# Kernel tuning notes

Measured on AMD Instinct MI355X. Metric: run time of the kernel, lower is better.

The kernel has to match this reference:

```python
import jax, jax.numpy as jnp
import numpy as np

DETER, STOCH, ACT, HID, OBS = 1024, 32, 6, 1024, 1024
B, T = 256, 64

def _lin(x, w, b):
    return x @ w.T + b

def setup_inputs() -> dict:
    key = jax.random.key(0)
    ks = iter(jax.random.split(key, 40))
    def p(shape, scale=0.02):
        return (jax.random.normal(next(ks), shape, dtype=jnp.float32) * scale)
    inp = {
        "obs": jax.random.normal(next(ks), (B, T, OBS), dtype=jnp.float32),
        "actions": jax.random.normal(next(ks), (B, T, ACT), dtype=jnp.float32),
        "eps_prior": jax.random.normal(next(ks), (B, T, STOCH), dtype=jnp.float32),
        "eps_post": jax.random.normal(next(ks), (B, T, STOCH), dtype=jnp.float32),
        # input_mlp
        "in_w1": p((HID, STOCH + ACT)), "in_b1": p((HID,)),
        "in_w2": p((HID, HID)), "in_b2": p((HID,)),
        # GRUCell (torch layout: r,z,n chunks)
        "gru_wih": p((3 * DETER, HID)), "gru_whh": p((3 * DETER, DETER)),
        "gru_bih": p((3 * DETER,)), "gru_bhh": p((3 * DETER,)),
        # prior
        "pr_w1": p((HID, DETER)), "pr_b1": p((HID,)),
        "pr_w2": p((HID, HID)), "pr_b2": p((HID,)),
        "pr_mw": p((STOCH, HID)), "pr_mb": p((STOCH,)),
        "pr_sw": p((STOCH, HID)), "pr_sb": p((STOCH,)),
        # posterior
        "po_w1": p((HID, DETER + OBS)), "po_b1": p((HID,)),
        "po_w2": p((HID, HID)), "po_b2": p((HID,)),
        "po_mw": p((STOCH, HID)), "po_mb": p((STOCH,)),
        "po_sw": p((STOCH, HID)), "po_sb": p((STOCH,)),
    }
    return inp

def _rollout(obs, actions, eps_prior, eps_post,
             in_w1, in_b1, in_w2, in_b2,
             gru_wih, gru_whh, gru_bih, gru_bhh,
             pr_w1, pr_b1, pr_w2, pr_b2, pr_mw, pr_mb, pr_sw, pr_sb,
             po_w1, po_b1, po_w2, po_b2, po_mw, po_mb, po_sw, po_sb):
    Bn = obs.shape[0]
    h0 = jnp.zeros((Bn, DETER), obs.dtype)
    z0 = jnp.zeros((Bn, STOCH), obs.dtype)
    a0 = jnp.zeros((Bn, ACT), obs.dtype)

    def step(carry, xs):
        h, z, prev_a = carry
        obs_t, act_t, ep, eq = xs
        x = jnp.concatenate([z, prev_a], axis=-1)
        x = jax.nn.relu(_lin(x, in_w1, in_b1))
        x = jax.nn.relu(_lin(x, in_w2, in_b2))
        # GRUCell
        gi = _lin(x, gru_wih, gru_bih)
        gh = _lin(h, gru_whh, gru_bhh)
        ir, iz, inn = jnp.split(gi, 3, axis=-1)
        hr, hz, hn = jnp.split(gh, 3, axis=-1)
        r = jax.nn.sigmoid(ir + hr)
        u = jax.nn.sigmoid(iz + hz)
        n = jnp.tanh(inn + r * hn)
        h_new = (1.0 - u) * n + u * h
        # prior
        px = jax.nn.relu(_lin(h_new, pr_w1, pr_b1))
        px = jax.nn.relu(_lin(px, pr_w2, pr_b2))
        p_mean = _lin(px, pr_mw, pr_mb)
        p_std = jnp.exp(jnp.clip(_lin(px, pr_sw, pr_sb), -5.0, 2.0))
        # posterior
        qx = jnp.concatenate([h_new, obs_t], axis=-1)
        qx = jax.nn.relu(_lin(qx, po_w1, po_b1))
        qx = jax.nn.relu(_lin(qx, po_w2, po_b2))
        q_mean = _lin(qx, po_mw, po_mb)
        q_std = jnp.exp(jnp.clip(_lin(qx, po_sw, po_sb), -5.0, 2.0))
        z_new = q_mean + q_std * eq
        feat = jnp.concatenate([h_new, z_new], axis=-1)
        return (h_new, z_new, act_t), (feat, p_mean, p_std, q_mean, q_std)

    xs = (jnp.swapaxes(obs, 0, 1), jnp.swapaxes(actions, 0, 1),
          jnp.swapaxes(eps_prior, 0, 1), jnp.swapaxes(eps_post, 0, 1))
    _, (feat, pm, ps, qm, qs) = jax.lax.scan(step, (h0, z0, a0), xs)
    to_bt = lambda a: jnp.swapaxes(a, 0, 1)  # [T,B,...] -> [B,T,...]
    return to_bt(feat), to_bt(pm), to_bt(ps), to_bt(qm), to_bt(qs)

def reference(obs, actions, eps_prior, eps_post,
              in_w1, in_b1, in_w2, in_b2,
              gru_wih, gru_whh, gru_bih, gru_bhh,
              pr_w1, pr_b1, pr_w2, pr_b2, pr_mw, pr_mb, pr_sw, pr_sb,
              po_w1, po_b1, po_w2, po_b2, po_mw, po_mb, po_sw, po_sb):
    return _rollout(obs, actions, eps_prior, eps_post,
                    in_w1, in_b1, in_w2, in_b2,
                    gru_wih, gru_whh, gru_bih, gru_bhh,
                    pr_w1, pr_b1, pr_w2, pr_b2, pr_mw, pr_mb, pr_sw, pr_sb,
                    po_w1, po_b1, po_w2, po_b2, po_mw, po_mb, po_sw, po_sb)
```

## Files before the change

### kernel.cpp

```cpp
#include <hip/hip_runtime.h>
#include <hip/hip_bf16.h>

#define B_   256
#define T_   64
#define OBS_ 1024
#define ACT_ 6
#define STO_ 32
#define HID_ 1024

using bf16 = __bf16;
typedef __attribute__((ext_vector_type(8))) __bf16 bf16x8;
typedef __attribute__((ext_vector_type(4))) float f32x4;

__device__ __forceinline__ f32x4 MF(bf16x8 a, bf16x8 b, f32x4 c) {
  return __builtin_amdgcn_mfma_f32_16x16x32_bf16(a, b, c, 0, 0, 0);
}

struct CvtArgs {
  const float *in_w2, *gru_wih, *gru_whh, *pr_w1, *pr_w2, *po_w1, *po_w2;
  const float *pr_mw, *pr_sw, *po_mw, *po_sw, *obs;
  bf16 *w_in2b, *w_wihb, *w_whhb, *w_pr1b, *w_pr2b, *w_po1hb, *w_po1ob, *w_po2b, *w_headb, *obsb;
};

__global__ void k_cvtall(CvtArgs a) {
  const int row = blockIdx.x;
  const float* src; bf16* dst;
  if      (row < 1024)  { src = a.in_w2   + (size_t)row * 1024;               dst = a.w_in2b  + (size_t)row * 1024; }
  else if (row < 4096)  { int r = row - 1024;  src = a.gru_wih + (size_t)r * 1024;        dst = a.w_wihb  + (size_t)r * 1024; }
  else if (row < 7168)  { int r = row - 4096;  src = a.gru_whh + (size_t)r * 1024;        dst = a.w_whhb  + (size_t)r * 1024; }
  else if (row < 8192)  { int r = row - 7168;  src = a.pr_w1   + (size_t)r * 1024;        dst = a.w_pr1b  + (size_t)r * 1024; }
  else if (row < 9216)  { int r = row - 8192;  src = a.pr_w2   + (size_t)r * 1024;        dst = a.w_pr2b  + (size_t)r * 1024; }
  else if (row < 10240) { int r = row - 9216;  src = a.po_w1   + (size_t)r * 2048;        dst = a.w_po1hb + (size_t)r * 1024; }
  else if (row < 11264) { int r = row - 10240; src = a.po_w1   + (size_t)r * 2048 + 1024; dst = a.w_po1ob + (size_t)r * 1024; }
  else if (row < 12288) { int r = row - 11264; src = a.po_w2   + (size_t)r * 1024;        dst = a.w_po2b  + (size_t)r * 1024; }
  else if (row < 12416) {
    int r = row - 12288;
    const float* hs[4] = { a.pr_mw, a.pr_sw, a.po_mw, a.po_sw };
    src = hs[r >> 5] + (size_t)(r & 31) * 1024;
    dst = a.w_headb + (size_t)r * 1024;
  }
  else { int r = row - 12416; src = a.obs + (size_t)r * 1024; dst = a.obsb + (size_t)r * 1024; }
  const int c = threadIdx.x * 4;
  float4 f = *(const float4*)(src + c);
  dst[c] = (bf16)f.x; dst[c + 1] = (bf16)f.y; dst[c + 2] = (bf16)f.z; dst[c + 3] = (bf16)f.w;
}

__global__ void k_init(const float* __restrict__ in_b1, bf16* __restrict__ x1b,
                       bf16* __restrict__ hbA, bf16* __restrict__ hbB,
                       float* __restrict__ hfA, float* __restrict__ hfB) {
  const int i = blockIdx.x * 256 + threadIdx.x;
  x1b[i] = (bf16)fmaxf(in_b1[i & 1023], 0.f);
  hbA[i] = (bf16)0.f; hbB[i] = (bf16)0.f;
  hfA[i] = 0.f; hfB[i] = 0.f;
}

struct GB2 {
  const bf16 *A1, *A2, *W1, *W2;
  const float* bias;
  bf16* out;
  int lda1, lda2, K1, kseg;
};

__global__ __launch_bounds__(256, 4) void k_l1(GB2 g0, GB2 g1, int s1) {
  GB2 g; int tile;
  if ((int)blockIdx.x < s1) { g = g0; tile = blockIdx.x; }
  else                      { g = g1; tile = blockIdx.x - s1; }
  __shared__ float sh[3 * 1056];
  const int tid = threadIdx.x, lane = tid & 63, kw = tid >> 6;
  const int l15 = lane & 15, kg = lane >> 4, kq = kg * 8, rq = kg * 4;
  const int m0 = (tile & 15) * 16, n0 = (tile >> 4) * 64;
  const int kb = kw * g.kseg;

  const bf16* __restrict__ ap;
  const bf16* __restrict__ wp;
  if (kb < g.K1) {
    ap = g.A1 + (size_t)(m0 + l15) * g.lda1 + kb + kq;
    wp = g.W1 + (size_t)(n0 + l15) * 1024 + kb + kq;
  } else {
    ap = g.A2 + (size_t)(m0 + l15) * g.lda2 + (kb - g.K1) + kq;
    wp = g.W2 + (size_t)(n0 + l15) * 1024 + (kb - g.K1) + kq;
  }
  f32x4 c0{0.f,0.f,0.f,0.f}, c1 = c0, c2 = c0, c3 = c0;
  #pragma unroll 8
  for (int k = 0; k < g.kseg; k += 32) {
    bf16x8 af = *(const bf16x8*)(ap + k);
    c0 = MF(af, *(const bf16x8*)(wp + k            ), c0);
    c1 = MF(af, *(const bf16x8*)(wp + 16 * 1024 + k), c1);
    c2 = MF(af, *(const bf16x8*)(wp + 32 * 1024 + k), c2);
    c3 = MF(af, *(const bf16x8*)(wp + 48 * 1024 + k), c3);
  }
  f32x4 cc[4] = {c0, c1, c2, c3};
  if (kw) {
    float* s = sh + (kw - 1) * 1056;
    #pragma unroll
    for (int t2 = 0; t2 < 4; ++t2)
      #pragma unroll
      for (int r = 0; r < 4; ++r)
        s[(rq + r) * 66 + t2 * 16 + l15] = cc[t2][r];
  }
  __syncthreads();
  if (kw == 0) {
    #pragma unroll
    for (int t2 = 0; t2 < 4; ++t2) {
      const int n = n0 + t2 * 16 + l15;
      const float bv = g.bias[n];
      #pragma unroll
      for (int r = 0; r < 4; ++r) {
        float v = cc[t2][r] + bv;
        #pragma unroll
        for (int s = 0; s < 3; ++s)
          v += sh[s * 1056 + (rq + r) * 66 + t2 * 16 + l15];
        g.out[(size_t)(m0 + rq + r) * 1024 + n] = (bf16)fmaxf(v, 0.f);
      }
    }
  }
}

__global__ __launch_bounds__(512, 2) void k_gru(
    const bf16* __restrict__ hbPrev, const float* __restrict__ hfPrev,
    bf16* __restrict__ hbCur, float* __restrict__ hfCur,
    const bf16* __restrict__ x2b, const bf16* __restrict__ wih,
    const bf16* __restrict__ whh, const float* __restrict__ bih,
    const float* __restrict__ bhh, float* __restrict__ feat, int t) {
  __shared__ float sh[4 * 1088];
  const int mt = blockIdx.x & 3, cs = blockIdx.x >> 2;
  const int tid = threadIdx.x, lane = tid & 63, wv = tid >> 6;
  const int msub = wv & 3, kw = wv >> 2;
  const int l15 = lane & 15, kg = lane >> 4, kq = kg * 8, rq = kg * 4;
  const int mrow = mt * 64 + msub * 16;
  const int c0 = cs * 16;
  const int kb = kw * 512;
  const size_t GOFF = (size_t)1024 * 1024;

  f32x4 ghR{0.f,0.f,0.f,0.f}, ghZ = ghR, ghN = ghR, giR = ghR, giZ = ghR, giN = ghR;
  {
    const bf16* __restrict__ ap = hbPrev + (size_t)(mrow + l15) * 1024 + kb + kq;
    const bf16* __restrict__ wr = whh + (size_t)(c0 + l15) * 1024 + kb + kq;
    #pragma unroll 4
    for (int k = 0; k < 512; k += 32) {
      bf16x8 af = *(const bf16x8*)(ap + k);
      ghR = MF(af, *(const bf16x8*)(wr + k           ), ghR);
      ghZ = MF(af, *(const bf16x8*)(wr + GOFF + k    ), ghZ);
      ghN = MF(af, *(const bf16x8*)(wr + 2 * GOFF + k), ghN);
    }
  }
  {
    const bf16* __restrict__ ap = x2b + (size_t)(mrow + l15) * 1024 + kb + kq;
    const bf16* __restrict__ wr = wih + (size_t)(c0 + l15) * 1024 + kb + kq;
    #pragma unroll 4
    for (int k = 0; k < 512; k += 32) {
      bf16x8 af = *(const bf16x8*)(ap + k);
      giR = MF(af, *(const bf16x8*)(wr + k           ), giR);
      giZ = MF(af, *(const bf16x8*)(wr + GOFF + k    ), giZ);
      giN = MF(af, *(const bf16x8*)(wr + 2 * GOFF + k), giN);
    }
  }
  f32x4 sR = ghR + giR, sZ = ghZ + giZ;
  if (kw) {
    float* s = sh + msub * 1088;
    #pragma unroll
    for (int r = 0; r < 4; ++r) {
      s[      (rq + r) * 17 + l15] = sR[r];
      s[272 + (rq + r) * 17 + l15] = sZ[r];
      s[544 + (rq + r) * 17 + l15] = giN[r];
      s[816 + (rq + r) * 17 + l15] = ghN[r];
    }
  }
  __syncthreads();
  if (kw == 0) {
    const int c = c0 + l15;
    const float bir = bih[c], biz = bih[1024 + c], bin_ = bih[2048 + c];
    const float bhr = bhh[c], bhz = bhh[1024 + c], bhn = bhh[2048 + c];
    const float* s = sh + msub * 1088;
    #pragma unroll
    for (int r = 0; r < 4; ++r) {
      const float vr  = sR[r]  + s[      (rq + r) * 17 + l15];
      const float vz  = sZ[r]  + s[272 + (rq + r) * 17 + l15];
      const float vin = giN[r] + s[544 + (rq + r) * 17 + l15];
      const float vhn = ghN[r] + s[816 + (rq + r) * 17 + l15];
      const int row = mrow + rq + r;
      float rr = vr + bir + bhr;
      float zz = vz + biz + bhz;
      rr = 1.f / (1.f + __expf(-rr));
      zz = 1.f / (1.f + __expf(-zz));
      const float nn = tanhf(vin + bin_ + rr * (vhn + bhn));
      const float h2 = (1.f - zz) * nn + zz * hfPrev[(size_t)row * 1024 + c];
      hbCur[(size_t)row * 1024 + c] = (bf16)h2;
      hfCur[(size_t)row * 1024 + c] = h2;
      feat[((size_t)row * T_ + t) * 1056 + c] = h2;
    }
  }
}

__global__ __launch_bounds__(1024, 1) void k_fin3(
    const bf16* __restrict__ p2b, const bf16* __restrict__ q2b,
    const bf16* __restrict__ whead, const bf16* __restrict__ win2,
    const float* __restrict__ pr_mb, const float* __restrict__ pr_sb,
    const float* __restrict__ po_mb, const float* __restrict__ po_sb,
    const float* __restrict__ b_in2,
    const float* __restrict__ eps, const float* __restrict__ act,
    const float* __restrict__ in_w1, const float* __restrict__ in_b1,
    float* __restrict__ pm, float* __restrict__ ps,
    float* __restrict__ qm, float* __restrict__ qs,
    float* __restrict__ feat, bf16* __restrict__ x2b, int t) {
  __shared__ float sh[12288];
  const int g = blockIdx.x >> 3, nt = blockIdx.x & 7, m0 = g * 16;
  const int tid = threadIdx.x, lane = tid & 63, wv = tid >> 6;
  const int l15 = lane & 15, kg = lane >> 4, kq = kg * 8, rq = kg * 4;
  float* zm = sh + 8448;
  float* zs = sh + 8960;
  float* zl = sh + 9472;
  float* al = sh + 9984;
  float* shE = sh + 10112;

  if (wv < 8) {
    const int kw = wv & 3, half = wv >> 2;
    const bf16* __restrict__ A = half ? q2b : p2b;
    f32x4 c0{0.f,0.f,0.f,0.f}, c1 = c0, c2 = c0, c3 = c0;
    const bf16* __restrict__ ap = A + (size_t)(m0 + l15) * 1024 + kw * 256 + kq;
    const bf16* __restrict__ wp = whead + (size_t)(half * 64 + l15) * 1024 + kw * 256 + kq;
    #pragma unroll
    for (int k = 0; k < 256; k += 32) {
      bf16x8 af = *(const bf16x8*)(ap + k);
      c0 = MF(af, *(const bf16x8*)(wp + k            ), c0);
      c1 = MF(af, *(const bf16x8*)(wp + 16 * 1024 + k), c1);
      c2 = MF(af, *(const bf16x8*)(wp + 32 * 1024 + k), c2);
      c3 = MF(af, *(const bf16x8*)(wp + 48 * 1024 + k), c3);
    }
    f32x4 cc[4] = {c0, c1, c2, c3};
    float* s = sh + wv * 1056;
    #pragma unroll
    for (int t2 = 0; t2 < 4; ++t2)
      #pragma unroll
      for (int r = 0; r < 4; ++r)
        s[(rq + r) * 66 + t2 * 16 + l15] = cc[t2][r];
  }
  if (tid >= 928 && tid < 1024) {
    const int idx = tid - 928, r = idx / ACT_, k = idx - r * ACT_;
    al[r * 8 + k] = act[((size_t)(m0 + r) * T_ + t) * ACT_ + k];
  }
  __syncthreads();

  #pragma unroll
  for (int rep = 0; rep < 2; ++rep) {
    const int idx = rep * 1024 + tid;
    const int r = idx >> 7, c = idx & 127;
    const int base = (c < 64) ? 0 : 4, cl = c & 63, j = c & 31;
    float v = sh[base * 1056 + r * 66 + cl] + sh[(base + 1) * 1056 + r * 66 + cl]
            + sh[(base + 2) * 1056 + r * 66 + cl] + sh[(base + 3) * 1056 + r * 66 + cl];
    const size_t ob = ((size_t)(m0 + r) * T_ + t) * STO_ + j;
    const int sel = c >> 5;
    if (sel == 0) {
      if (nt == 0) pm[ob] = v + pr_mb[j];
    } else if (sel == 1) {
      if (nt == 0) ps[ob] = __expf(fminf(fmaxf(v + pr_sb[j], -5.f), 2.f));
    } else if (sel == 2) {
      const float x = v + po_mb[j];
      if (nt == 0) qm[ob] = x;
      zm[r * 32 + j] = x;
    } else {
      const float x = __expf(fminf(fmaxf(v + po_sb[j], -5.f), 2.f));
      if (nt == 0) qs[ob] = x;
      zs[r * 32 + j] = x;
    }
  }
  __syncthreads();

  if (tid < 512) {
    const int r = tid >> 5, j = tid & 31;
    const float z = zm[r * 32 + j] + zs[r * 32 + j] * eps[((size_t)(m0 + r) * T_ + t) * STO_ + j];
    zl[r * 32 + j] = z;
    if (nt == 0) feat[((size_t)(m0 + r) * T_ + t) * 1056 + 1024 + j] = z;
  }
  __syncthreads();

  {
    char* x1c = (char*)sh;
    const int n = tid;
    const float* w = in_w1 + (size_t)n * 38;
    float wreg[38];
    #pragma unroll
    for (int j = 0; j < 38; ++j) wreg[j] = w[j];
    const float bn = in_b1[n];
    const int chunk = n >> 3, sub = (n & 7) * 2;
    #pragma unroll 2
    for (int r = 0; r < 16; ++r) {
      float a = bn;
      #pragma unroll
      for (int k = 0; k < STO_; ++k) a = fmaf(zl[r * 32 + k], wreg[k], a);
      #pragma unroll
      for (int k = 0; k < ACT_; ++k) a = fmaf(al[r * 8 + k], wreg[32 + k], a);
      *(bf16*)(x1c + r * 2048 + ((chunk ^ (r & 7)) << 4) + sub) = (bf16)fmaxf(a, 0.f);
    }
  }
  __syncthreads();

  {
    const char* x1c = (const char*)sh;
    const int nfrag = wv & 7, kw2 = wv >> 3;
    const int col = nt * 128 + nfrag * 16 + l15;
    f32x4 e0{0.f,0.f,0.f,0.f};
    const bf16* __restrict__ wp = win2 + (size_t)col * 1024 + kw2 * 512 + kq;
    #pragma unroll 4
    for (int k = 0; k < 512; k += 32) {
      const int chunk = (kw2 * 512 + k + kq) >> 3;
      bf16x8 af = *(const bf16x8*)(x1c + l15 * 2048 + ((chunk ^ (l15 & 7)) << 4));
      e0 = MF(af, *(const bf16x8*)(wp + k), e0);
    }
    if (kw2) {
      float* s = shE + nfrag * 272;
      #pragma unroll
      for (int r = 0; r < 4; ++r) s[(rq + r) * 17 + l15] = e0[r];
    }
    __syncthreads();
    if (kw2 == 0) {
      const float* s = shE + nfrag * 272;
      const float bv = b_in2[col];
      #pragma unroll
      for (int r = 0; r < 4; ++r) {
        const float v = e0[r] + s[(rq + r) * 17 + l15] + bv;
        x2b[(size_t)(m0 + rq + r) * 1024 + col] = (bf16)fmaxf(v, 0.f);
      }
    }
  }
}

extern "C" void kernel_launch(void* const* d_in, const int* in_sizes, int n_in,
                              void* d_out, int out_size, void* d_ws, size_t ws_size,
                              hipStream_t stream) {
  (void)in_sizes; (void)n_in; (void)out_size; (void)ws_size;
  const float* obs      = (const float*)d_in[0];
  const float* actions  = (const float*)d_in[1];
  const float* eps_post = (const float*)d_in[3];
  const float* in_w1 = (const float*)d_in[4];
  const float* in_b1 = (const float*)d_in[5];
  const float* in_w2 = (const float*)d_in[6];
  const float* in_b2 = (const float*)d_in[7];
  const float* gru_wih = (const float*)d_in[8];
  const float* gru_whh = (const float*)d_in[9];
  const float* gru_bih = (const float*)d_in[10];
  const float* gru_bhh = (const float*)d_in[11];
  const float* pr_w1 = (const float*)d_in[12];
  const float* pr_b1 = (const float*)d_in[13];
  const float* pr_w2 = (const float*)d_in[14];
  const float* pr_b2 = (const float*)d_in[15];
  const float* pr_mw = (const float*)d_in[16];
  const float* pr_mb = (const float*)d_in[17];
  const float* pr_sw = (const float*)d_in[18];
  const float* pr_sb = (const float*)d_in[19];
  const float* po_w1 = (const float*)d_in[20];
  const float* po_b1 = (const float*)d_in[21];
  const float* po_w2 = (const float*)d_in[22];
  const float* po_b2 = (const float*)d_in[23];
  const float* po_mw = (const float*)d_in[24];
  const float* po_mb = (const float*)d_in[25];
  const float* po_sw = (const float*)d_in[26];
  const float* po_sb = (const float*)d_in[27];

  float* feat = (float*)d_out;
  float* pm = feat + (size_t)B_ * T_ * 1056;
  float* ps = pm + (size_t)B_ * T_ * STO_;
  float* qm = ps + (size_t)B_ * T_ * STO_;
  float* qs = qm + (size_t)B_ * T_ * STO_;

  char* wp_ = (char*)d_ws;
  auto carve = [&](size_t bytes) -> void* {
    void* r = (void*)wp_;
    wp_ += (bytes + 255) & ~(size_t)255;
    return r;
  };
  bf16* w_in2b  = (bf16*)carve((size_t)HID_ * HID_ * 2);
  bf16* w_wihb  = (bf16*)carve((size_t)3 * HID_ * HID_ * 2);
  bf16* w_whhb  = (bf16*)carve((size_t)3 * HID_ * HID_ * 2);
  bf16* w_pr1b  = (bf16*)carve((size_t)HID_ * HID_ * 2);
  bf16* w_pr2b  = (bf16*)carve((size_t)HID_ * HID_ * 2);
  bf16* w_po1hb = (bf16*)carve((size_t)HID_ * HID_ * 2);
  bf16* w_po1ob = (bf16*)carve((size_t)HID_ * OBS_ * 2);
  bf16* w_po2b  = (bf16*)carve((size_t)HID_ * HID_ * 2);
  bf16* w_headb = (bf16*)carve((size_t)128 * HID_ * 2);
  bf16* obsb    = (bf16*)carve((size_t)B_ * T_ * OBS_ * 2);
  bf16* x1b = (bf16*)carve((size_t)B_ * HID_ * 2);
  bf16* x2b = (bf16*)carve((size_t)B_ * HID_ * 2);
  bf16* hbA = (bf16*)carve((size_t)B_ * HID_ * 2);
  bf16* hbB = (bf16*)carve((size_t)B_ * HID_ * 2);
  bf16* p1b = (bf16*)carve((size_t)B_ * HID_ * 2);
  bf16* q1b = (bf16*)carve((size_t)B_ * HID_ * 2);
  bf16* p2b = (bf16*)carve((size_t)B_ * HID_ * 2);
  bf16* q2b = (bf16*)carve((size_t)B_ * HID_ * 2);
  float* hfA = (float*)carve((size_t)B_ * HID_ * 4);
  float* hfB = (float*)carve((size_t)B_ * HID_ * 4);

  CvtArgs ca = { in_w2, gru_wih, gru_whh, pr_w1, pr_w2, po_w1, po_w2,
                 pr_mw, pr_sw, po_mw, po_sw, obs,
                 w_in2b, w_wihb, w_whhb, w_pr1b, w_pr2b, w_po1hb, w_po1ob, w_po2b, w_headb, obsb };
  k_cvtall<<<dim3(28800), dim3(256), 0, stream>>>(ca);
  k_init<<<dim3(1024), dim3(256), 0, stream>>>(in_b1, x1b, hbA, hbB, hfA, hfB);

  GB2 dummy = {};
  GB2 g_x2i = { x1b, nullptr, w_in2b, nullptr, in_b2, x2b, 1024, 0, 1024, 256 };
  k_l1<<<dim3(256), dim3(256), 0, stream>>>(g_x2i, dummy, 256);

  for (int t = 0; t < T_; ++t) {
    bf16* hbCur = (t & 1) ? hbB : hbA;
    bf16* hbPrev = (t & 1) ? hbA : hbB;
    float* hfCur = (t & 1) ? hfB : hfA;
    float* hfPrev = (t & 1) ? hfA : hfB;

    k_gru<<<dim3(256), dim3(512), 0, stream>>>(
        hbPrev, hfPrev, hbCur, hfCur, x2b, w_wihb, w_whhb, gru_bih, gru_bhh, feat, t);

    GB2 g_pr1 = { hbCur, nullptr, w_pr1b, nullptr, pr_b1, p1b, 1024, 0, 1024, 256 };
    GB2 g_q1  = { hbCur, obsb + (size_t)t * 1024, w_po1hb, w_po1ob, po_b1, q1b,
                  1024, T_ * 1024, 1024, 512 };
    k_l1<<<dim3(512), dim3(256), 0, stream>>>(g_pr1, g_q1, 256);

    GB2 g_pr2 = { p1b, nullptr, w_pr2b, nullptr, pr_b2, p2b, 1024, 0, 1024, 256 };
    GB2 g_po2 = { q1b, nullptr, w_po2b, nullptr, po_b2, q2b, 1024, 0, 1024, 256 };
    k_l1<<<dim3(512), dim3(256), 0, stream>>>(g_pr2, g_po2, 256);

    k_fin3<<<dim3(128), dim3(1024), 0, stream>>>(
        p2b, q2b, w_headb, w_in2b, pr_mb, pr_sb, po_mb, po_sb, in_b2,
        eps_post, actions, in_w1, in_b1, pm, ps, qm, qs, feat, x2b, t);
  }
}
```

Measured before the change: 5.730 ms.

## Fuse posterior layer-2 into final kernel and defer prior heads off critical path

```diff
diff --git a/kernel.cpp b/kernel.cpp
--- a/kernel.cpp
+++ b/kernel.cpp
@@ -61,11 +61,7 @@
   int lda1, lda2, K1, kseg;
 };
 
-__global__ __launch_bounds__(256, 4) void k_l1(GB2 g0, GB2 g1, int s1) {
-  GB2 g; int tile;
-  if ((int)blockIdx.x < s1) { g = g0; tile = blockIdx.x; }
-  else                      { g = g1; tile = blockIdx.x - s1; }
-  __shared__ float sh[3 * 1056];
+__device__ __forceinline__ void gb2_run(const GB2& g, int tile, float* sh) {
   const int tid = threadIdx.x, lane = tid & 63, kw = tid >> 6;
   const int l15 = lane & 15, kg = lane >> 4, kq = kg * 8, rq = kg * 4;
   const int m0 = (tile & 15) * 16, n0 = (tile >> 4) * 64;
@@ -114,6 +110,64 @@
       }
     }
   }
+}
+
+__global__ __launch_bounds__(256, 4) void k_l1(GB2 g0, GB2 g1, int s1) {
+  __shared__ float sh[3 * 1056];
+  if ((int)blockIdx.x < s1) gb2_run(g0, blockIdx.x, sh);
+  else                      gb2_run(g1, blockIdx.x - s1, sh);
+}
+
+__device__ __forceinline__ void heads_p_run(
+    int g2, int tlab, const bf16* __restrict__ p2b, const bf16* __restrict__ whead,
+    const float* __restrict__ pr_mb, const float* __restrict__ pr_sb,
+    float* __restrict__ pm, float* __restrict__ ps, float* shp) {
+  const int tid = threadIdx.x, lane = tid & 63, wv = tid >> 6;
+  const int l15 = lane & 15, kg = lane >> 4, kq = kg * 8;
+  const int m0 = g2 * 16;
+  {
+    f32x4 c{0.f, 0.f, 0.f, 0.f};
+    const bf16* __restrict__ ap = p2b + (size_t)(m0 + l15) * 1024 + kq;
+    const bf16* __restrict__ wp = whead + (size_t)(wv * 16 + l15) * 1024 + kq;
+    #pragma unroll 4
+    for (int k = 0; k < 1024; k += 32) {
+      bf16x8 af = *(const bf16x8*)(ap + k);
+      c = MF(af, *(const bf16x8*)(wp + k), c);
+    }
+    #pragma unroll
+    for (int r = 0; r < 4; ++r)
+      shp[(kg * 4 + r) * 64 + wv * 16 + l15] = c[r];
+  }
+  __syncthreads();
+  #pragma unroll
+  for (int rep = 0; rep < 4; ++rep) {
+    const int idx = rep * 256 + tid;
+    const int r = idx >> 6, c = idx & 63;
+    const float v = shp[r * 64 + c];
+    const size_t ob = ((size_t)(m0 + r) * T_ + tlab) * STO_ + (c & 31);
+    if (c < 32) pm[ob] = v + pr_mb[c];
+    else        ps[ob] = __expf(fminf(fmaxf(v + pr_sb[c - 32], -5.f), 2.f));
+  }
+}
+
+__global__ __launch_bounds__(256, 4) void k_l2(
+    GB2 g0, GB2 g1,
+    const bf16* __restrict__ p2b, const bf16* __restrict__ whead,
+    const float* __restrict__ pr_mb, const float* __restrict__ pr_sb,
+    float* __restrict__ pm, float* __restrict__ ps, int t) {
+  __shared__ float sh[3 * 1056];
+  const int bid = blockIdx.x;
+  if (bid < 256)      gb2_run(g0, bid, sh);
+  else if (bid < 512) gb2_run(g1, bid - 256, sh);
+  else if (t > 0)     heads_p_run(bid - 512, t - 1, p2b, whead, pr_mb, pr_sb, pm, ps, sh);
+}
+
+__global__ __launch_bounds__(256, 4) void k_hp(
+    const bf16* __restrict__ p2b, const bf16* __restrict__ whead,
+    const float* __restrict__ pr_mb, const float* __restrict__ pr_sb,
+    float* __restrict__ pm, float* __restrict__ ps) {
+  __shared__ float sh[1024];
+  heads_p_run(blockIdx.x, T_ - 1, p2b, whead, pr_mb, pr_sb, pm, ps, sh);
 }
 
 __global__ __launch_bounds__(512, 2) void k_gru(
@@ -192,35 +246,57 @@
   }
 }
 
-__global__ __launch_bounds__(1024, 1) void k_fin3(
-    const bf16* __restrict__ p2b, const bf16* __restrict__ q2b,
+__global__ __launch_bounds__(1024, 1) void k_fin4(
+    const bf16* __restrict__ q1b, const bf16* __restrict__ p1b,
+    const bf16* __restrict__ w_po2, const float* __restrict__ b_po2,
+    const bf16* __restrict__ w_pr2, const float* __restrict__ b_pr2,
+    bf16* __restrict__ p2b,
     const bf16* __restrict__ whead, const bf16* __restrict__ win2,
-    const float* __restrict__ pr_mb, const float* __restrict__ pr_sb,
     const float* __restrict__ po_mb, const float* __restrict__ po_sb,
     const float* __restrict__ b_in2,
     const float* __restrict__ eps, const float* __restrict__ act,
     const float* __restrict__ in_w1, const float* __restrict__ in_b1,
-    float* __restrict__ pm, float* __restrict__ ps,
     float* __restrict__ qm, float* __restrict__ qs,
     float* __restrict__ feat, bf16* __restrict__ x2b, int t) {
-  __shared__ float sh[12288];
-  const int g = blockIdx.x >> 3, nt = blockIdx.x & 7, m0 = g * 16;
-  const int tid = threadIdx.x, lane = tid & 63, wv = tid >> 6;
+  __shared__ float sh[12032];
+  const int bid = blockIdx.x, tid = threadIdx.x;
+  const int lane = tid & 63, wv = tid >> 6;
   const int l15 = lane & 15, kg = lane >> 4, kq = kg * 8, rq = kg * 4;
-  float* zm = sh + 8448;
-  float* zs = sh + 8960;
-  float* zl = sh + 9472;
-  float* al = sh + 9984;
-  float* shE = sh + 10112;
-
-  if (wv < 8) {
-    const int kw = wv & 3, half = wv >> 2;
-    const bf16* __restrict__ A = half ? q2b : p2b;
+
+  if (bid >= 128) {
+    const int idx = bid - 128, mt = idx & 15, nc = idx >> 4;
+    const int m0 = mt * 16, cb = nc * 256 + wv * 16;
+    f32x4 c{0.f, 0.f, 0.f, 0.f};
+    const bf16* __restrict__ ap = p1b + (size_t)(m0 + l15) * 1024 + kq;
+    const bf16* __restrict__ wp = w_pr2 + (size_t)(cb + l15) * 1024 + kq;
+    #pragma unroll 4
+    for (int k = 0; k < 1024; k += 32) {
+      bf16x8 af = *(const bf16x8*)(ap + k);
+      c = MF(af, *(const bf16x8*)(wp + k), c);
+    }
+    const float bv = b_pr2[cb + l15];
+    #pragma unroll
+    for (int r = 0; r < 4; ++r) {
+      const float v = fmaxf(c[r] + bv, 0.f);
+      p2b[(size_t)(m0 + kg * 4 + r) * 1024 + cb + l15] = (bf16)v;
+    }
+    return;
+  }
+
+  const int g = bid >> 3, nt = bid & 7, m0 = g * 16;
+  float* hq  = sh + 8192;
+  float* zl  = sh + 9216;
+  float* al  = sh + 9728;
+  float* shE = sh + 9856;
+  char* ldsb = (char*)sh;
+
+  {
+    const int cw = wv * 64;
     f32x4 c0{0.f,0.f,0.f,0.f}, c1 = c0, c2 = c0, c3 = c0;
-    const bf16* __restrict__ ap = A + (size_t)(m0 + l15) * 1024 + kw * 256 + kq;
-    const bf16* __restrict__ wp = whead + (size_t)(half * 64 + l15) * 1024 + kw * 256 + kq;
-    #pragma unroll
-    for (int k = 0; k < 256; k += 32) {
+    const bf16* __restrict__ ap = q1b + (size_t)(m0 + l15) * 1024 + kq;
+    const bf16* __restrict__ wp = w_po2 + (size_t)(cw + l15) * 1024 + kq;
+    #pragma unroll 4
+    for (int k = 0; k < 1024; k += 32) {
       bf16x8 af = *(const bf16x8*)(ap + k);
       c0 = MF(af, *(const bf16x8*)(wp + k            ), c0);
       c1 = MF(af, *(const bf16x8*)(wp + 16 * 1024 + k), c1);
@@ -228,54 +304,60 @@
       c3 = MF(af, *(const bf16x8*)(wp + 48 * 1024 + k), c3);
     }
     f32x4 cc[4] = {c0, c1, c2, c3};
-    float* s = sh + wv * 1056;
-    #pragma unroll
-    for (int t2 = 0; t2 < 4; ++t2)
-      #pragma unroll
-      for (int r = 0; r < 4; ++r)
-        s[(rq + r) * 66 + t2 * 16 + l15] = cc[t2][r];
-  }
-  if (tid >= 928 && tid < 1024) {
-    const int idx = tid - 928, r = idx / ACT_, k = idx - r * ACT_;
-    al[r * 8 + k] = act[((size_t)(m0 + r) * T_ + t) * ACT_ + k];
-  }
-  __syncthreads();
-
-  #pragma unroll
-  for (int rep = 0; rep < 2; ++rep) {
-    const int idx = rep * 1024 + tid;
-    const int r = idx >> 7, c = idx & 127;
-    const int base = (c < 64) ? 0 : 4, cl = c & 63, j = c & 31;
-    float v = sh[base * 1056 + r * 66 + cl] + sh[(base + 1) * 1056 + r * 66 + cl]
-            + sh[(base + 2) * 1056 + r * 66 + cl] + sh[(base + 3) * 1056 + r * 66 + cl];
-    const size_t ob = ((size_t)(m0 + r) * T_ + t) * STO_ + j;
-    const int sel = c >> 5;
-    if (sel == 0) {
-      if (nt == 0) pm[ob] = v + pr_mb[j];
-    } else if (sel == 1) {
-      if (nt == 0) ps[ob] = __expf(fminf(fmaxf(v + pr_sb[j], -5.f), 2.f));
-    } else if (sel == 2) {
-      const float x = v + po_mb[j];
-      if (nt == 0) qm[ob] = x;
-      zm[r * 32 + j] = x;
-    } else {
-      const float x = __expf(fminf(fmaxf(v + po_sb[j], -5.f), 2.f));
-      if (nt == 0) qs[ob] = x;
-      zs[r * 32 + j] = x;
-    }
+    #pragma unroll
+    for (int t2 = 0; t2 < 4; ++t2) {
+      const int dcol = cw + t2 * 16 + l15;
+      const float bv = b_po2[dcol];
+      const int chunk = dcol >> 3, sub = (dcol & 7) * 2;
+      #pragma unroll
+      for (int r = 0; r < 4; ++r) {
+        const int drow = kg * 4 + r;
+        const float v = fmaxf(cc[t2][r] + bv, 0.f);
+        *(bf16*)(ldsb + drow * 2048 + ((chunk ^ (drow & 7)) << 4) + sub) = (bf16)v;
+      }
+    }
+  }
+  if (tid >= 928) {
+    const int idx2 = tid - 928;
+    if (idx2 < 96) {
+      const int r = idx2 / ACT_, k = idx2 - r * ACT_;
+      al[r * 8 + k] = act[((size_t)(m0 + r) * T_ + t) * ACT_ + k];
+    }
+  }
+  __syncthreads();
+
+  if (wv < 4) {
+    const int hc = wv * 16;
+    f32x4 c{0.f, 0.f, 0.f, 0.f};
+    const bf16* __restrict__ wp = whead + (size_t)(64 + hc + l15) * 1024 + kq;
+    #pragma unroll 4
+    for (int k = 0; k < 1024; k += 32) {
+      const int chunk = (k + kq) >> 3;
+      bf16x8 af = *(const bf16x8*)(ldsb + l15 * 2048 + ((chunk ^ (l15 & 7)) << 4));
+      c = MF(af, *(const bf16x8*)(wp + k), c);
+    }
+    #pragma unroll
+    for (int r = 0; r < 4; ++r)
+      hq[(kg * 4 + r) * 64 + hc + l15] = c[r];
   }
   __syncthreads();
 
   if (tid < 512) {
     const int r = tid >> 5, j = tid & 31;
-    const float z = zm[r * 32 + j] + zs[r * 32 + j] * eps[((size_t)(m0 + r) * T_ + t) * STO_ + j];
+    const size_t ob = ((size_t)(m0 + r) * T_ + t) * STO_ + j;
+    const float vm = hq[r * 64 + j] + po_mb[j];
+    const float vs = __expf(fminf(fmaxf(hq[r * 64 + 32 + j] + po_sb[j], -5.f), 2.f));
+    const float z = vm + vs * eps[ob];
     zl[r * 32 + j] = z;
-    if (nt == 0) feat[((size_t)(m0 + r) * T_ + t) * 1056 + 1024 + j] = z;
+    if (nt == 0) {
+      qm[ob] = vm;
+      qs[ob] = vs;
+      feat[((size_t)(m0 + r) * T_ + t) * 1056 + 1024 + j] = z;
+    }
   }
   __syncthreads();
 
   {
-    char* x1c = (char*)sh;
     const int n = tid;
     const float* w = in_w1 + (size_t)n * 38;
     float wreg[38];
@@ -290,21 +372,20 @@
       for (int k = 0; k < STO_; ++k) a = fmaf(zl[r * 32 + k], wreg[k], a);
       #pragma unroll
       for (int k = 0; k < ACT_; ++k) a = fmaf(al[r * 8 + k], wreg[32 + k], a);
-      *(bf16*)(x1c + r * 2048 + ((chunk ^ (r & 7)) << 4) + sub) = (bf16)fmaxf(a, 0.f);
+      *(bf16*)(ldsb + r * 2048 + ((chunk ^ (r & 7)) << 4) + sub) = (bf16)fmaxf(a, 0.f);
     }
   }
   __syncthreads();
 
   {
-    const char* x1c = (const char*)sh;
     const int nfrag = wv & 7, kw2 = wv >> 3;
     const int col = nt * 128 + nfrag * 16 + l15;
-    f32x4 e0{0.f,0.f,0.f,0.f};
+    f32x4 e0{0.f, 0.f, 0.f, 0.f};
     const bf16* __restrict__ wp = win2 + (size_t)col * 1024 + kw2 * 512 + kq;
     #pragma unroll 4
     for (int k = 0; k < 512; k += 32) {
       const int chunk = (kw2 * 512 + k + kq) >> 3;
-      bf16x8 af = *(const bf16x8*)(x1c + l15 * 2048 + ((chunk ^ (l15 & 7)) << 4));
+      bf16x8 af = *(const bf16x8*)(ldsb + l15 * 2048 + ((chunk ^ (l15 & 7)) << 4));
       e0 = MF(af, *(const bf16x8*)(wp + k), e0);
     }
     if (kw2) {
@@ -386,7 +467,6 @@
   bf16* p1b = (bf16*)carve((size_t)B_ * HID_ * 2);
   bf16* q1b = (bf16*)carve((size_t)B_ * HID_ * 2);
   bf16* p2b = (bf16*)carve((size_t)B_ * HID_ * 2);
-  bf16* q2b = (bf16*)carve((size_t)B_ * HID_ * 2);
   float* hfA = (float*)carve((size_t)B_ * HID_ * 4);
   float* hfB = (float*)carve((size_t)B_ * HID_ * 4);
 
@@ -409,17 +489,17 @@
     k_gru<<<dim3(256), dim3(512), 0, stream>>>(
         hbPrev, hfPrev, hbCur, hfCur, x2b, w_wihb, w_whhb, gru_bih, gru_bhh, feat, t);
 
-    GB2 g_pr1 = { hbCur, nullptr, w_pr1b, nullptr, pr_b1, p1b, 1024, 0, 1024, 256 };
     GB2 g_q1  = { hbCur, obsb + (size_t)t * 1024, w_po1hb, w_po1ob, po_b1, q1b,
                   1024, T_ * 1024, 1024, 512 };
-    k_l1<<<dim3(512), dim3(256), 0, stream>>>(g_pr1, g_q1, 256);
-
-    GB2 g_pr2 = { p1b, nullptr, w_pr2b, nullptr, pr_b2, p2b, 1024, 0, 1024, 256 };
-    GB2 g_po2 = { q1b, nullptr, w_po2b, nullptr, po_b2, q2b, 1024, 0, 1024, 256 };
-    k_l1<<<dim3(512), dim3(256), 0, stream>>>(g_pr2, g_po2, 256);
-
-    k_fin3<<<dim3(128), dim3(1024), 0, stream>>>(
-        p2b, q2b, w_headb, w_in2b, pr_mb, pr_sb, po_mb, po_sb, in_b2,
-        eps_post, actions, in_w1, in_b1, pm, ps, qm, qs, feat, x2b, t);
-  }
-}
+    GB2 g_pr1 = { hbCur, nullptr, w_pr1b, nullptr, pr_b1, p1b, 1024, 0, 1024, 256 };
+    k_l2<<<dim3(528), dim3(256), 0, stream>>>(
+        g_q1, g_pr1, p2b, w_headb, pr_mb, pr_sb, pm, ps, t);
+
+    k_fin4<<<dim3(192), dim3(1024), 0, stream>>>(
+        q1b, p1b, w_po2b, po_b2, w_pr2b, pr_b2, p2b,
+        w_headb, w_in2b, po_mb, po_sb, in_b2,
+        eps_post, actions, in_w1, in_b1, qm, qs, feat, x2b, t);
+  }
+
+  k_hp<<<dim3(16), dim3(256), 0, stream>>>(p2b, w_headb, pr_mb, pr_sb, pm, ps);
+}
```

Result: slower. 9.454 ms (+65.0%).
